# Optimization experiments

Hardware: AMD Instinct MI355X
Metric: run time of the kernel (lower is better)

## Reference

```python
import jax, jax.numpy as jnp
import numpy as np

D = 2048          # n_embd
H = 4 * D         # hidden_size
B, S = 4, 2048


def _make_masks(seed=0):
    rng = np.random.default_rng(seed)
    # mask1: for each group of 4 output rows, keep 2 of 4 rows (whole rows)
    mask1 = np.zeros((H, D), dtype=np.float32)
    for i in range(0, H, 4):
        keep = rng.permutation(4)[:2] + i
        mask1[keep, :] = 1.0
    # mask2: for each group of 4 input columns, keep 2 of 4 columns
    mask2 = np.zeros((D, H), dtype=np.float32)
    for i in range(0, H, 4):
        keep = rng.permutation(4)[:2] + i
        mask2[:, keep] = 1.0
    return jnp.asarray(mask1), jnp.asarray(mask2)


def setup_inputs() -> dict:
    key = jax.random.key(0)
    k_x, k_w1, k_w2 = jax.random.split(key, 3)
    x = jax.random.normal(k_x, (B, S, D), dtype=jnp.float32)
    # Kaiming-uniform-ish init like nn.Linear defaults
    w1 = jax.random.uniform(k_w1, (H, D), dtype=jnp.float32, minval=-1.0, maxval=1.0) / np.sqrt(D)
    w2 = jax.random.uniform(k_w2, (D, H), dtype=jnp.float32, minval=-1.0, maxval=1.0) / np.sqrt(H)
    mask1, mask2 = _make_masks()
    return {"x": x, "w1": w1, "w2": w2, "mask1": mask1, "mask2": mask2}


def reference(x, w1, w2, mask1, mask2):
    # sparse_multiply is elementwise mask application on the weights
    sw1 = w1 * mask1                      # [H, D]
    sw2 = w2 * mask2                      # [D, H]
    h = jnp.einsum('bsd,hd->bsh', x, sw1) # F.linear(x, sw1)
    h = jax.nn.gelu(h, approximate=False) # torch F.gelu default = exact erf
    out = jnp.einsum('bsh,dh->bsd', h, sw2)
    return out
```

## Files before the change

kernel.cpp:

```cpp
#include <hip/hip_runtime.h>
#include <hip/hip_bf16.h>

typedef __bf16 bf16_t;
typedef __bf16 bf16x8 __attribute__((ext_vector_type(8)));
typedef float f32x4 __attribute__((ext_vector_type(4)));

__device__ __forceinline__ unsigned short f32_to_bf16_rn(float f) {
  unsigned u = __float_as_uint(f);
  u += 0x7fffu + ((u >> 16) & 1u);
  return (unsigned short)(u >> 16);
}

__device__ __forceinline__ ushort4 cvt4(float4 v) {
  ushort4 o;
  o.x = f32_to_bf16_rn(v.x);
  o.y = f32_to_bf16_rn(v.y);
  o.z = f32_to_bf16_rn(v.z);
  o.w = f32_to_bf16_rn(v.w);
  return o;
}

__device__ __forceinline__ float gelu_exact(float x) {
  return 0.5f * x * (1.0f + erff(x * 0.7071067811865475f));
}

#define GLDS16(g, l)                                                          \
  __builtin_amdgcn_global_load_lds(                                           \
      (const __attribute__((address_space(1))) void*)(g),                     \
      (__attribute__((address_space(3))) void*)(l), 16, 0, 0)

__global__ void build_idx_kernel(const float* __restrict__ mask1,
                                 const float* __restrict__ mask2,
                                 int* __restrict__ idx, int* __restrict__ meta,
                                 int H, int D) {
  __shared__ int sums[1024];
  const int t = threadIdx.x;
  int flags[8];
  int tot = 0;
#pragma unroll
  for (int u = 0; u < 8; ++u) {
    int j = t * 8 + u;
    int f = (mask1[(long long)j * D] != 0.0f) && (mask2[j] != 0.0f);
    flags[u] = f;
    tot += f;
  }
  sums[t] = tot;
  __syncthreads();
  for (int off = 1; off < 1024; off <<= 1) {
    int v = (t >= off) ? sums[t - off] : 0;
    __syncthreads();
    sums[t] += v;
    __syncthreads();
  }
  int pos = sums[t] - tot;
#pragma unroll
  for (int u = 0; u < 8; ++u) {
    if (flags[u]) idx[pos++] = t * 8 + u;
  }
  if (t == 1023) {
    int count = sums[1023];
    meta[0] = count;
    meta[1] = (count + 127) & ~127;
  }
}

__global__ void prep_kernel(const float* __restrict__ x,
                            const float* __restrict__ w1,
                            const int* __restrict__ idx,
                            const int* __restrict__ meta,
                            unsigned short* __restrict__ xb,
                            unsigned short* __restrict__ w1c, int D) {
  const int nx = 4194304;
  const int nw1 = 2097152;
  const int count = meta[0];
  for (int i = blockIdx.x * 256 + threadIdx.x; i < nx + nw1; i += 2048 * 256) {
    if (i < nx) {
      ((ushort4*)xb)[i] = cvt4(((const float4*)x)[i]);
    } else {
      int q = i - nx;
      int k = q >> 9;
      int d4 = (q & 511) << 2;
      ushort4 o = {0, 0, 0, 0};
      if (k < count)
        o = cvt4(*(const float4*)(w1 + (long long)idx[k] * D + d4));
      *(ushort4*)(w1c + (long long)k * D + d4) = o;
    }
  }
}

#define POOLG 2048
#define W2BLKS 512

template <int EPI, int DOW2>
__global__ __launch_bounds__(256, 3) void gemm_pool_kernel(
    const bf16_t* __restrict__ A, const bf16_t* __restrict__ B,
    void* __restrict__ Cout, long long ldA, long long ldB, long long ldC,
    int Kfix, int ncolFix, const int* __restrict__ meta,
    const float* __restrict__ w2src, const int* __restrict__ idx,
    unsigned short* __restrict__ w2c, int H) {
  if (DOW2 && blockIdx.x >= POOLG) {
    const int nq = 2097152;
    const int count = meta[0];
    for (int q = (blockIdx.x - POOLG) * 256 + threadIdx.x; q < nq;
         q += W2BLKS * 256) {
      int n = q >> 10;
      int k4 = (q & 1023) << 2;
      ushort4 o = {0, 0, 0, 0};
      const float* src = w2src + (long long)n * H;
#pragma unroll
      for (int u = 0; u < 4; ++u) {
        int k = k4 + u;
        unsigned short v = 0;
        if (k < count) v = f32_to_bf16_rn(src[idx[k]]);
        ((unsigned short*)&o)[u] = v;
      }
      *(ushort4*)(w2c + (long long)n * 4096 + k4) = o;
    }
    return;
  }

  const int kpad = meta[1];
  const int K = (EPI == 0) ? kpad : Kfix;
  const int ncol = (EPI == 1) ? (kpad >> 6) : ncolFix;
  const int ntiles = ncol << 6;

  __shared__ bf16_t As[128 * 128];
  __shared__ bf16_t Bs[64 * 128];

  const int tid = threadIdx.x;
  const int l = tid & 63;
  const int w = tid >> 6;
  const int wm = w >> 1;
  const int wn = w & 1;

  const int srow = tid >> 4;
  const int sgl = ((tid & 15) ^ ((tid >> 4) & 7)) * 8;

  const int fr = l & 15;

  for (int tau = blockIdx.x; tau < ntiles; tau += POOLG) {
    const int row = tau & 63;
    const int col = tau >> 6;
    const long long brow = (long long)row * 128;
    const long long bcol = (long long)col * 64;

    const bf16_t* Ag = A + (brow + srow) * ldA + sgl;
    const bf16_t* Bg = B + (bcol + srow) * ldB + sgl;

    f32x4 acc[4][2];
#pragma unroll
    for (int m = 0; m < 4; ++m)
#pragma unroll
      for (int n = 0; n < 2; ++n) acc[m][n] = (f32x4){0.f, 0.f, 0.f, 0.f};

    for (int k0 = 0; k0 < K; k0 += 128) {
#pragma unroll
      for (int a = 0; a < 8; ++a)
        GLDS16(Ag + a * 16 * ldA + k0, &As[a * 2048 + tid * 8]);
#pragma unroll
      for (int b = 0; b < 4; ++b)
        GLDS16(Bg + b * 16 * ldB + k0, &Bs[b * 2048 + tid * 8]);
      __syncthreads();
#pragma unroll
      for (int kk = 0; kk < 4; ++kk) {
        const int gp = ((((l >> 4) + 4 * kk) ^ (l & 7)) * 8);
        bf16x8 af[4], bfr[2];
#pragma unroll
        for (int m = 0; m < 4; ++m)
          af[m] = *(const bf16x8*)(&As[(wm * 64 + m * 16 + fr) * 128 + gp]);
#pragma unroll
        for (int n = 0; n < 2; ++n)
          bfr[n] = *(const bf16x8*)(&Bs[(wn * 32 + n * 16 + fr) * 128 + gp]);
#pragma unroll
        for (int m = 0; m < 4; ++m)
#pragma unroll
          for (int n = 0; n < 2; ++n)
            acc[m][n] = __builtin_amdgcn_mfma_f32_16x16x32_bf16(
                af[m], bfr[n], acc[m][n], 0, 0, 0);
      }
      __syncthreads();
    }

    const int orow = wm * 64 + (l >> 4) * 4;
    const int ocol = wn * 32 + fr;
#pragma unroll
    for (int m = 0; m < 4; ++m)
#pragma unroll
      for (int n = 0; n < 2; ++n)
#pragma unroll
        for (int r = 0; r < 4; ++r) {
          long long rr = brow + orow + m * 16 + r;
          long long cc = bcol + ocol + n * 16;
          float v = acc[m][n][r];
          if (EPI == 1) {
            ((unsigned short*)Cout)[rr * ldC + cc] =
                f32_to_bf16_rn(gelu_exact(v));
          } else {
            ((float*)Cout)[rr * ldC + cc] = v;
          }
        }
  }
}

extern "C" void kernel_launch(void* const* d_in, const int* in_sizes, int n_in,
                              void* d_out, int out_size, void* d_ws,
                              size_t ws_size, hipStream_t stream) {
  const float* x = (const float*)d_in[0];
  const float* w1 = (const float*)d_in[1];
  const float* w2 = (const float*)d_in[2];
  const float* mask1 = (const float*)d_in[3];
  const float* mask2 = (const float*)d_in[4];
  float* out = (float*)d_out;

  const int D = 2048, H = 8192, M = 8192;
  const int KP = 4096;

  char* ws = (char*)d_ws;
  unsigned short* xb = (unsigned short*)ws;
  unsigned short* w1c = xb + (size_t)M * D;
  unsigned short* w2c = w1c + (size_t)KP * D;
  unsigned short* hb = w2c + (size_t)D * KP;
  int* idx = (int*)(hb + (size_t)M * KP);
  int* meta = idx + KP;

  build_idx_kernel<<<1, 1024, 0, stream>>>(mask1, mask2, idx, meta, H, D);

  prep_kernel<<<2048, 256, 0, stream>>>(x, w1, idx, meta, xb, w1c, D);

  gemm_pool_kernel<1, 1><<<POOLG + W2BLKS, 256, 0, stream>>>(
      (const bf16_t*)xb, (const bf16_t*)w1c, hb, (long long)D, (long long)D,
      (long long)KP, D, 0, meta, w2, idx, w2c, H);

  gemm_pool_kernel<0, 0><<<POOLG, 256, 0, stream>>>(
      (const bf16_t*)hb, (const bf16_t*)w2c, out, (long long)KP,
      (long long)KP, (long long)D, 0, 32, meta, nullptr, nullptr, nullptr, H);
}
```

Before: 272.3 us.

## Pre-tile operands into MFMA fragment layout and load directly from global

Prep kernels now write x, compressed w1, w2 and the hidden activations in a blocked 16x32 fragment layout, so each lane's MFMA operand is one contiguous 16-byte load. The GEMM drops LDS staging and barriers entirely and reads fragments straight from global memory, with occupancy raised to 4 blocks. This removes LDS traffic and syncs, but it loses cross-wave data reuse through shared memory, relies on L2/cache hits, and exposes global latency without explicit pipelining. The compressed w1 conversion work is also trimmed to the padded count.

Result: slower. 396.8 us (+45.7%).

```diff
diff --git a/kernel.cpp b/kernel.cpp
--- a/kernel.cpp
+++ b/kernel.cpp
@@ -23,11 +23,6 @@
 __device__ __forceinline__ float gelu_exact(float x) {
   return 0.5f * x * (1.0f + erff(x * 0.7071067811865475f));
 }
-
-#define GLDS16(g, l)                                                          \
-  __builtin_amdgcn_global_load_lds(                                           \
-      (const __attribute__((address_space(1))) void*)(g),                     \
-      (__attribute__((address_space(3))) void*)(l), 16, 0, 0)
 
 __global__ void build_idx_kernel(const float* __restrict__ mask1,
                                  const float* __restrict__ mask2,
@@ -64,6 +59,7 @@
   }
 }
 
+
 __global__ void prep_kernel(const float* __restrict__ x,
                             const float* __restrict__ w1,
                             const int* __restrict__ idx,
@@ -71,19 +67,25 @@
                             unsigned short* __restrict__ xb,
                             unsigned short* __restrict__ w1c, int D) {
   const int nx = 4194304;
-  const int nw1 = 2097152;
   const int count = meta[0];
+  const int kpad = meta[1];
+  const int nw1 = kpad << 9;
   for (int i = blockIdx.x * 256 + threadIdx.x; i < nx + nw1; i += 2048 * 256) {
     if (i < nx) {
-      ((ushort4*)xb)[i] = cvt4(((const float4*)x)[i]);
+      int row = i >> 9;
+      int d0 = (i & 511) << 2;
+      ushort4 o = cvt4(((const float4*)x)[i]);
+      *(ushort4*)(xb + (size_t)((row >> 4) * 64 + (d0 >> 5)) * 512 +
+                  ((d0 >> 3) & 3) * 128 + (row & 15) * 8 + (d0 & 7)) = o;
     } else {
       int q = i - nx;
       int k = q >> 9;
-      int d4 = (q & 511) << 2;
+      int d0 = (q & 511) << 2;
       ushort4 o = {0, 0, 0, 0};
       if (k < count)
-        o = cvt4(*(const float4*)(w1 + (long long)idx[k] * D + d4));
-      *(ushort4*)(w1c + (long long)k * D + d4) = o;
+        o = cvt4(*(const float4*)(w1 + (long long)idx[k] * D + d0));
+      *(ushort4*)(w1c + (size_t)((k >> 4) * 64 + (d0 >> 5)) * 512 +
+                  ((d0 >> 3) & 3) * 128 + (k & 15) * 8 + (d0 & 7)) = o;
     }
   }
 }
@@ -92,60 +94,60 @@
 #define W2BLKS 512
 
 template <int EPI, int DOW2>
-__global__ __launch_bounds__(256, 3) void gemm_pool_kernel(
+__global__ __launch_bounds__(256, 4) void gemm_direct_kernel(
     const bf16_t* __restrict__ A, const bf16_t* __restrict__ B,
-    void* __restrict__ Cout, long long ldA, long long ldB, long long ldC,
-    int Kfix, int ncolFix, const int* __restrict__ meta,
-    const float* __restrict__ w2src, const int* __restrict__ idx,
-    unsigned short* __restrict__ w2c, int H) {
+    void* __restrict__ Cout, int NKBfix, int Kfix, int ncolFix,
+    const int* __restrict__ meta, const float* __restrict__ w2src,
+    const int* __restrict__ idx, unsigned short* __restrict__ w2c, int H) {
   if (DOW2 && blockIdx.x >= POOLG) {
-    const int nq = 2097152;
     const int count = meta[0];
+    const int kpad = meta[1];
+    const int NKB2 = kpad >> 5;
+    const int kq = kpad >> 2;
+    const int nq = 2048 * kq;
     for (int q = (blockIdx.x - POOLG) * 256 + threadIdx.x; q < nq;
          q += W2BLKS * 256) {
-      int n = q >> 10;
-      int k4 = (q & 1023) << 2;
+      int n = q / kq;
+      int k0 = (q - n * kq) << 2;
       ushort4 o = {0, 0, 0, 0};
       const float* src = w2src + (long long)n * H;
 #pragma unroll
       for (int u = 0; u < 4; ++u) {
-        int k = k4 + u;
+        int k = k0 + u;
         unsigned short v = 0;
         if (k < count) v = f32_to_bf16_rn(src[idx[k]]);
         ((unsigned short*)&o)[u] = v;
       }
-      *(ushort4*)(w2c + (long long)n * 4096 + k4) = o;
+      *(ushort4*)(w2c + (size_t)((n >> 4) * NKB2 + (k0 >> 5)) * 512 +
+                  ((k0 >> 3) & 3) * 128 + (n & 15) * 8 + (k0 & 7)) = o;
     }
     return;
   }
 
   const int kpad = meta[1];
-  const int K = (EPI == 0) ? kpad : Kfix;
-  const int ncol = (EPI == 1) ? (kpad >> 6) : ncolFix;
+  const int K = EPI ? Kfix : kpad;
+  const int NKB = K >> 5;
+  const int NKBa = EPI ? NKBfix : (kpad >> 5);
+  const int NKBb = EPI ? NKBfix : (kpad >> 5);
+  const int NKBh = kpad >> 5;
+  const int ncol = EPI ? (kpad >> 6) : ncolFix;
   const int ntiles = ncol << 6;
-
-  __shared__ bf16_t As[128 * 128];
-  __shared__ bf16_t Bs[64 * 128];
 
   const int tid = threadIdx.x;
   const int l = tid & 63;
   const int w = tid >> 6;
   const int wm = w >> 1;
   const int wn = w & 1;
-
-  const int srow = tid >> 4;
-  const int sgl = ((tid & 15) ^ ((tid >> 4) & 7)) * 8;
-
-  const int fr = l & 15;
+  const int loff = l * 8;
 
   for (int tau = blockIdx.x; tau < ntiles; tau += POOLG) {
     const int row = tau & 63;
-    const int col = tau >> 6;
-    const long long brow = (long long)row * 128;
-    const long long bcol = (long long)col * 64;
-
-    const bf16_t* Ag = A + (brow + srow) * ldA + sgl;
-    const bf16_t* Bg = B + (bcol + srow) * ldB + sgl;
+    const int colI = tau >> 6;
+    const int amb = row * 8 + wm * 4;
+    const int bnb = colI * 4 + wn * 2;
+
+    const bf16_t* Ap = A + (size_t)amb * NKBa * 512 + loff;
+    const bf16_t* Bp = B + (size_t)bnb * NKBb * 512 + loff;
 
     f32x4 acc[4][2];
 #pragma unroll
@@ -153,52 +155,51 @@
 #pragma unroll
       for (int n = 0; n < 2; ++n) acc[m][n] = (f32x4){0.f, 0.f, 0.f, 0.f};
 
-    for (int k0 = 0; k0 < K; k0 += 128) {
-#pragma unroll
-      for (int a = 0; a < 8; ++a)
-        GLDS16(Ag + a * 16 * ldA + k0, &As[a * 2048 + tid * 8]);
-#pragma unroll
-      for (int b = 0; b < 4; ++b)
-        GLDS16(Bg + b * 16 * ldB + k0, &Bs[b * 2048 + tid * 8]);
-      __syncthreads();
-#pragma unroll
-      for (int kk = 0; kk < 4; ++kk) {
-        const int gp = ((((l >> 4) + 4 * kk) ^ (l & 7)) * 8);
-        bf16x8 af[4], bfr[2];
-#pragma unroll
-        for (int m = 0; m < 4; ++m)
-          af[m] = *(const bf16x8*)(&As[(wm * 64 + m * 16 + fr) * 128 + gp]);
+#pragma unroll 2
+    for (int kb = 0; kb < NKB; ++kb) {
+      bf16x8 a[4], b[2];
+#pragma unroll
+      for (int m = 0; m < 4; ++m)
+        a[m] = *(const bf16x8*)(Ap + ((size_t)m * NKBa + kb) * 512);
+#pragma unroll
+      for (int n = 0; n < 2; ++n)
+        b[n] = *(const bf16x8*)(Bp + ((size_t)n * NKBb + kb) * 512);
+#pragma unroll
+      for (int m = 0; m < 4; ++m)
 #pragma unroll
         for (int n = 0; n < 2; ++n)
-          bfr[n] = *(const bf16x8*)(&Bs[(wn * 32 + n * 16 + fr) * 128 + gp]);
-#pragma unroll
-        for (int m = 0; m < 4; ++m)
-#pragma unroll
-          for (int n = 0; n < 2; ++n)
-            acc[m][n] = __builtin_amdgcn_mfma_f32_16x16x32_bf16(
-                af[m], bfr[n], acc[m][n], 0, 0, 0);
-      }
-      __syncthreads();
-    }
-
-    const int orow = wm * 64 + (l >> 4) * 4;
-    const int ocol = wn * 32 + fr;
-#pragma unroll
-    for (int m = 0; m < 4; ++m)
-#pragma unroll
-      for (int n = 0; n < 2; ++n)
-#pragma unroll
-        for (int r = 0; r < 4; ++r) {
-          long long rr = brow + orow + m * 16 + r;
-          long long cc = bcol + ocol + n * 16;
-          float v = acc[m][n][r];
-          if (EPI == 1) {
-            ((unsigned short*)Cout)[rr * ldC + cc] =
-                f32_to_bf16_rn(gelu_exact(v));
-          } else {
-            ((float*)Cout)[rr * ldC + cc] = v;
-          }
+          acc[m][n] = __builtin_amdgcn_mfma_f32_16x16x32_bf16(a[m], b[n],
+                                                              acc[m][n], 0, 0, 0);
+    }
+
+    const int lr = (l >> 4) * 4;
+    const int lc = l & 15;
+    if (EPI == 1) {
+      unsigned short* hb = (unsigned short*)Cout;
+#pragma unroll
+      for (int m = 0; m < 4; ++m)
+#pragma unroll
+        for (int n = 0; n < 2; ++n) {
+          unsigned short* hp =
+              hb + (size_t)((amb + m) * NKBh + colI * 2 + wn) * 512 +
+              (n * 2 + (lc >> 3)) * 128 + (lc & 7);
+#pragma unroll
+          for (int r = 0; r < 4; ++r)
+            hp[(lr + r) * 8] = f32_to_bf16_rn(gelu_exact(acc[m][n][r]));
         }
+    } else {
+      float* o = (float*)Cout;
+      const long long r0 = (long long)row * 128 + wm * 64;
+      const int c0 = colI * 64 + wn * 32;
+#pragma unroll
+      for (int m = 0; m < 4; ++m)
+#pragma unroll
+        for (int n = 0; n < 2; ++n)
+#pragma unroll
+          for (int r = 0; r < 4; ++r)
+            o[(r0 + m * 16 + lr + r) * 2048 + c0 + n * 16 + lc] =
+                acc[m][n][r];
+    }
   }
 }
 
@@ -227,11 +228,11 @@
 
   prep_kernel<<<2048, 256, 0, stream>>>(x, w1, idx, meta, xb, w1c, D);
 
-  gemm_pool_kernel<1, 1><<<POOLG + W2BLKS, 256, 0, stream>>>(
-      (const bf16_t*)xb, (const bf16_t*)w1c, hb, (long long)D, (long long)D,
-      (long long)KP, D, 0, meta, w2, idx, w2c, H);
-
-  gemm_pool_kernel<0, 0><<<POOLG, 256, 0, stream>>>(
-      (const bf16_t*)hb, (const bf16_t*)w2c, out, (long long)KP,
-      (long long)KP, (long long)D, 0, 32, meta, nullptr, nullptr, nullptr, H);
-}
+  gemm_direct_kernel<1, 1><<<POOLG + W2BLKS, 256, 0, stream>>>(
+      (const bf16_t*)xb, (const bf16_t*)w1c, hb, 64, D, 0, meta, w2, idx, w2c,
+      H);
+
+  gemm_direct_kernel<0, 0><<<POOLG, 256, 0, stream>>>(
+      (const bf16_t*)hb, (const bf16_t*)w2c, out, 0, 0, 32, meta, nullptr,
+      nullptr, nullptr, H);
+}
```

## Switch GEMM tiles to 128x128 with K=64 steps and staggered K start

Applied to the files above, without the earlier changes.

The GEMM tile grows from 128x64 to 128x128 output with a 64-wide K slice. Each wave now computes 4x4 MFMA fragments, which raises arithmetic intensity per LDS load, and LDS drops to 32KB so occupancy can go to 4 blocks. Block groups start their K loop at staggered phases to spread memory traffic across the A and B rows, and the second GEMM launches 1024 blocks with 16 columns to match. The prep kernel also stops converting w1 rows beyond the padded count. Risks include higher register pressure from the 16 accumulators under launch_bounds 4, and more barriers from the shorter K steps.

Result: faster. 239.6 us (median of 2 runs) (-12.0%).

```diff
diff --git a/kernel.cpp b/kernel.cpp
--- a/kernel.cpp
+++ b/kernel.cpp
@@ -71,8 +71,9 @@
                             unsigned short* __restrict__ xb,
                             unsigned short* __restrict__ w1c, int D) {
   const int nx = 4194304;
-  const int nw1 = 2097152;
   const int count = meta[0];
+  const int kpad = meta[1];
+  const int nw1 = kpad << 9;
   for (int i = blockIdx.x * 256 + threadIdx.x; i < nx + nw1; i += 2048 * 256) {
     if (i < nx) {
       ((ushort4*)xb)[i] = cvt4(((const float4*)x)[i]);
@@ -92,7 +93,7 @@
 #define W2BLKS 512
 
 template <int EPI, int DOW2>
-__global__ __launch_bounds__(256, 3) void gemm_pool_kernel(
+__global__ __launch_bounds__(256, 4) void gemm_pool_kernel(
     const bf16_t* __restrict__ A, const bf16_t* __restrict__ B,
     void* __restrict__ Cout, long long ldA, long long ldB, long long ldC,
     int Kfix, int ncolFix, const int* __restrict__ meta,
@@ -121,11 +122,13 @@
 
   const int kpad = meta[1];
   const int K = (EPI == 0) ? kpad : Kfix;
-  const int ncol = (EPI == 1) ? (kpad >> 6) : ncolFix;
+  const int ncol = (EPI == 1) ? (kpad >> 7) : ncolFix;
   const int ntiles = ncol << 6;
-
-  __shared__ bf16_t As[128 * 128];
-  __shared__ bf16_t Bs[64 * 128];
+  const int NT = K >> 6;
+  const int phase = ((blockIdx.x >> 8) & 3) * (NT >> 2);
+
+  __shared__ bf16_t As[128 * 64];
+  __shared__ bf16_t Bs[128 * 64];
 
   const int tid = threadIdx.x;
   const int l = tid & 63;
@@ -133,48 +136,54 @@
   const int wm = w >> 1;
   const int wn = w & 1;
 
-  const int srow = tid >> 4;
-  const int sgl = ((tid & 15) ^ ((tid >> 4) & 7)) * 8;
+  const int srow = tid >> 3;
+  const int sg = ((tid & 7) ^ ((tid >> 3) & 7)) * 8;
 
   const int fr = l & 15;
+  const int gA = (l >> 4) ^ (l & 7);
 
   for (int tau = blockIdx.x; tau < ntiles; tau += POOLG) {
     const int row = tau & 63;
     const int col = tau >> 6;
     const long long brow = (long long)row * 128;
-    const long long bcol = (long long)col * 64;
-
-    const bf16_t* Ag = A + (brow + srow) * ldA + sgl;
-    const bf16_t* Bg = B + (bcol + srow) * ldB + sgl;
-
-    f32x4 acc[4][2];
+    const long long bcol = (long long)col * 128;
+
+    const bf16_t* Ag = A + (brow + srow) * ldA + sg;
+    const bf16_t* Bg = B + (bcol + srow) * ldB + sg;
+
+    f32x4 acc[4][4];
 #pragma unroll
     for (int m = 0; m < 4; ++m)
 #pragma unroll
-      for (int n = 0; n < 2; ++n) acc[m][n] = (f32x4){0.f, 0.f, 0.f, 0.f};
-
-    for (int k0 = 0; k0 < K; k0 += 128) {
-#pragma unroll
-      for (int a = 0; a < 8; ++a)
-        GLDS16(Ag + a * 16 * ldA + k0, &As[a * 2048 + tid * 8]);
-#pragma unroll
-      for (int b = 0; b < 4; ++b)
-        GLDS16(Bg + b * 16 * ldB + k0, &Bs[b * 2048 + tid * 8]);
+      for (int n = 0; n < 4; ++n) acc[m][n] = (f32x4){0.f, 0.f, 0.f, 0.f};
+
+    for (int it = 0; it < NT; ++it) {
+      int t = it + phase;
+      if (t >= NT) t -= NT;
+      const int k0 = t << 6;
+      GLDS16(Ag + k0, &As[tid * 8]);
+      GLDS16(Ag + 32 * ldA + k0, &As[2048 + tid * 8]);
+      GLDS16(Ag + 64 * ldA + k0, &As[4096 + tid * 8]);
+      GLDS16(Ag + 96 * ldA + k0, &As[6144 + tid * 8]);
+      GLDS16(Bg + k0, &Bs[tid * 8]);
+      GLDS16(Bg + 32 * ldB + k0, &Bs[2048 + tid * 8]);
+      GLDS16(Bg + 64 * ldB + k0, &Bs[4096 + tid * 8]);
+      GLDS16(Bg + 96 * ldB + k0, &Bs[6144 + tid * 8]);
       __syncthreads();
 #pragma unroll
-      for (int kk = 0; kk < 4; ++kk) {
-        const int gp = ((((l >> 4) + 4 * kk) ^ (l & 7)) * 8);
-        bf16x8 af[4], bfr[2];
+      for (int kk = 0; kk < 2; ++kk) {
+        const int gp = (gA ^ (kk * 4)) * 8;
+        bf16x8 af[4], bfr[4];
 #pragma unroll
         for (int m = 0; m < 4; ++m)
-          af[m] = *(const bf16x8*)(&As[(wm * 64 + m * 16 + fr) * 128 + gp]);
-#pragma unroll
-        for (int n = 0; n < 2; ++n)
-          bfr[n] = *(const bf16x8*)(&Bs[(wn * 32 + n * 16 + fr) * 128 + gp]);
+          af[m] = *(const bf16x8*)(&As[(wm * 64 + m * 16 + fr) * 64 + gp]);
+#pragma unroll
+        for (int n = 0; n < 4; ++n)
+          bfr[n] = *(const bf16x8*)(&Bs[(wn * 64 + n * 16 + fr) * 64 + gp]);
 #pragma unroll
         for (int m = 0; m < 4; ++m)
 #pragma unroll
-          for (int n = 0; n < 2; ++n)
+          for (int n = 0; n < 4; ++n)
             acc[m][n] = __builtin_amdgcn_mfma_f32_16x16x32_bf16(
                 af[m], bfr[n], acc[m][n], 0, 0, 0);
       }
@@ -182,11 +191,11 @@
     }
 
     const int orow = wm * 64 + (l >> 4) * 4;
-    const int ocol = wn * 32 + fr;
+    const int ocol = wn * 64 + fr;
 #pragma unroll
     for (int m = 0; m < 4; ++m)
 #pragma unroll
-      for (int n = 0; n < 2; ++n)
+      for (int n = 0; n < 4; ++n)
 #pragma unroll
         for (int r = 0; r < 4; ++r) {
           long long rr = brow + orow + m * 16 + r;
@@ -231,7 +240,7 @@
       (const bf16_t*)xb, (const bf16_t*)w1c, hb, (long long)D, (long long)D,
       (long long)KP, D, 0, meta, w2, idx, w2c, H);
 
-  gemm_pool_kernel<0, 0><<<POOLG, 256, 0, stream>>>(
+  gemm_pool_kernel<0, 0><<<1024, 256, 0, stream>>>(
       (const bf16_t*)hb, (const bf16_t*)w2c, out, (long long)KP,
-      (long long)KP, (long long)D, 0, 32, meta, nullptr, nullptr, nullptr, H);
-}
+      (long long)KP, (long long)D, 0, 16, meta, nullptr, nullptr, nullptr, H);
+}
```
